# Optimization experiments

Hardware: AMD Instinct MI355X
Metric: run time of the kernel (lower is better)

The kernel has to match this reference:

```python
import jax, jax.numpy as jnp
import numpy as np


def setup_inputs() -> dict:
    key = jax.random.key(0)
    k1, k2, k3 = jax.random.split(key, 3)
    B, D = 16, 512
    lengths = np.array([1024 + 64 * i for i in range(B)], dtype=np.int64)  # ragged lens, max 1984
    N = int(lengths.sum())  # 24064 packed tokens
    h = jax.random.normal(k1, (N, D), dtype=jnp.float32)
    W = jax.random.normal(k2, (D, D), dtype=jnp.float32) / np.sqrt(D)
    b = jax.random.normal(k3, (D,), dtype=jnp.float32) * 0.01
    return {
        "h": h,
        "W": W,
        "b": b,
        "text_len_tensor": jnp.asarray(lengths),
        "max_len": int(lengths.max()),
    }


def reference(h, W, b, text_len_tensor, max_len):
    # h: [N, D] packed utterance features; text_len_tensor: [B] segment lengths.
    N, D = h.shape
    x = h @ W.T + b  # nn.Linear
    # Segment start offsets and padded gather indices [B, Lmax]
    offsets = jnp.concatenate(
        [jnp.zeros((1,), text_len_tensor.dtype), jnp.cumsum(text_len_tensor)[:-1]]
    )
    pos = jnp.arange(max_len)
    idx = offsets[:, None] + pos[None, :]
    mask = pos[None, :] < text_len_tensor[:, None]  # [B, Lmax] valid-token mask
    idx_c = jnp.clip(idx, 0, N - 1)
    z = h[idx_c] * mask[..., None]  # padded raw features  [B, Lmax, D]
    y = x[idx_c] * mask[..., None]  # padded projected     [B, Lmax, D]
    # Per-segment attention: scores[i, j] = z_i . y_j within each segment
    scores = jnp.einsum('bld,bmd->blm', z, y)
    scores = jnp.where(mask[:, None, :], scores, -1e9)  # mask invalid keys
    probs = jax.nn.softmax(scores, axis=-1)
    out = jnp.einsum('blm,bmd->bld', probs, z) * mask[..., None]
    # Scatter padded result back to packed layout (padding rows contribute zeros)
    ret = jnp.zeros_like(h).at[idx_c.reshape(-1)].add(out.reshape(-1, D))
    return ret
```

## Files before the change

kernel.cpp:

```cpp
#include <hip/hip_runtime.h>
#include <math.h>

#define D 512
#define AS1 __attribute__((address_space(1)))
#define AS3 __attribute__((address_space(3)))

typedef _Float16 f16x8 __attribute__((ext_vector_type(8)));
typedef float f32x4 __attribute__((ext_vector_type(4)));

__global__ __launch_bounds__(256) void transpose_kernel(
    const float* __restrict__ h, _Float16* __restrict__ zTb, int N)
{
    __shared__ float tile[64][65];
    const int t0 = blockIdx.x * 64;
    const int d0 = blockIdx.y * 64;
    const int tid = threadIdx.x;
    const int r0 = tid >> 4;
    const int c0 = (tid & 15) * 4;
    #pragma unroll
    for (int k = 0; k < 4; k++) {
        int r = r0 + k * 16;
        float4 v = *(const float4*)(h + (size_t)(t0 + r) * D + d0 + c0);
        tile[r][c0] = v.x; tile[r][c0+1] = v.y; tile[r][c0+2] = v.z; tile[r][c0+3] = v.w;
    }
    __syncthreads();
    const int g = (t0 >> 5) + (c0 >> 5);
    const int kk = c0 & 31;
    const int kg = kk >> 3;
    const int sub = kk & 7;
    #pragma unroll
    for (int k = 0; k < 4; k++) {
        int dd = d0 + r0 + k * 16;
        int kks = ((kg + (dd >> 1)) & 3) * 8 + sub;
        union { _Float16 hh[4]; uint2 u2; } pk;
        #pragma unroll
        for (int i = 0; i < 4; i++) pk.hh[i] = (_Float16)tile[c0 + i][r0 + k * 16];
        *(uint2*)(zTb + (size_t)g * 16384 + dd * 32 + kks) = pk.u2;
    }
}

__global__ __launch_bounds__(256) void linear_mfma(
    const float* __restrict__ h, const float* __restrict__ W,
    const float* __restrict__ bias, _Float16* __restrict__ x16, int N)
{
    __shared__ _Float16 sA[128 * 72];
    __shared__ _Float16 sB[128 * 72];
    const int tid  = threadIdx.x;
    const int m0 = blockIdx.x * 128;
    const int n0 = blockIdx.y * 128;
    const int wave = tid >> 6, lane = tid & 63;
    const int l15 = lane & 15, quad = lane >> 4;
    const int wm = (wave >> 1) * 64, wn = (wave & 1) * 64;

    f32x4 acc[4][4];
    #pragma unroll
    for (int mi = 0; mi < 4; mi++)
        #pragma unroll
        for (int ni = 0; ni < 4; ni++) acc[mi][ni] = (f32x4){0.f,0.f,0.f,0.f};

    for (int k0 = 0; k0 < D; k0 += 64) {
        __syncthreads();
        #pragma unroll
        for (int i = 0; i < 8; i++) {
            int idx = tid + 256 * i;
            int row = idx >> 4;
            int c4  = (idx & 15) * 4;
            float4 va = *(const float4*)(h + (size_t)(m0 + row) * D + k0 + c4);
            float4 vb = *(const float4*)(W + (size_t)(n0 + row) * D + k0 + c4);
            union { _Float16 hh[4]; uint2 u2; } pa, pb;
            pa.hh[0] = (_Float16)va.x; pa.hh[1] = (_Float16)va.y;
            pa.hh[2] = (_Float16)va.z; pa.hh[3] = (_Float16)va.w;
            pb.hh[0] = (_Float16)vb.x; pb.hh[1] = (_Float16)vb.y;
            pb.hh[2] = (_Float16)vb.z; pb.hh[3] = (_Float16)vb.w;
            *(uint2*)(sA + row * 72 + c4) = pa.u2;
            *(uint2*)(sB + row * 72 + c4) = pb.u2;
        }
        __syncthreads();
        #pragma unroll
        for (int kc = 0; kc < 2; kc++) {
            f16x8 a[4], b[4];
            #pragma unroll
            for (int mi = 0; mi < 4; mi++)
                a[mi] = *(const f16x8*)(sA + (wm + mi*16 + l15)*72 + kc*32 + quad*8);
            #pragma unroll
            for (int ni = 0; ni < 4; ni++)
                b[ni] = *(const f16x8*)(sB + (wn + ni*16 + l15)*72 + kc*32 + quad*8);
            #pragma unroll
            for (int mi = 0; mi < 4; mi++)
                #pragma unroll
                for (int ni = 0; ni < 4; ni++)
                    acc[mi][ni] = __builtin_amdgcn_mfma_f32_16x16x32_f16(a[mi], b[ni], acc[mi][ni], 0, 0, 0);
        }
    }
    float bv[4];
    #pragma unroll
    for (int ni = 0; ni < 4; ni++) bv[ni] = bias[n0 + wn + ni*16 + l15];
    #pragma unroll
    for (int mi = 0; mi < 4; mi++)
        #pragma unroll
        for (int ni = 0; ni < 4; ni++)
            #pragma unroll
            for (int r = 0; r < 4; r++) {
                int row = m0 + wm + mi*16 + quad*4 + r;
                x16[(size_t)row * D + n0 + wn + ni*16 + l15] = (_Float16)(acc[mi][ni][r] + bv[ni]);
            }
}

__global__ __launch_bounds__(256, 2) void attn9_kernel(
    const float* __restrict__ h, const _Float16* __restrict__ x16,
    const _Float16* __restrict__ zTb, const int* __restrict__ lens,
    float* __restrict__ out, int N, int B)
{
    __shared__ __align__(16) unsigned char smem[71168];
    _Float16* ybuf = (_Float16*)smem;
    _Float16* zbuf = (_Float16*)(smem + 33280);
    _Float16* pbuf = (_Float16*)(smem + 66048);

    const int is64 = (lens[1] == 0 && lens[3] == 0) ? 1 : 0;

    int seg = -1, tile = 0;
    if (B == 16) {
        const int xcd = blockIdx.x & 7;
        const int idx = blockIdx.x >> 3;
        const int sL = 15 - xcd, sS = xcd;
        const int LL = is64 ? lens[2 * sL] : lens[sL];
        const int LS = is64 ? lens[2 * sS] : lens[sS];
        const int ntL = (LL + 63) >> 6;
        const int ntS = (LS + 63) >> 6;
        if (idx < ntL)            { seg = sL; tile = idx; }
        else if (idx < ntL + ntS) { seg = sS; tile = idx - ntL; }
        else return;
    } else {
        int blk = blockIdx.x;
        int acc = 0;
        for (int t = 0; t < B; t++) {
            int s = B - 1 - t;
            int Ls = is64 ? lens[2 * s] : lens[s];
            int nt = (Ls + 63) >> 6;
            if (seg < 0 && blk < acc + nt) { seg = s; tile = blk - acc; }
            acc += nt;
        }
        if (seg < 0) return;
    }
    int off = 0;
    for (int t = 0; t < seg; t++) off += is64 ? lens[2 * t] : lens[t];
    const int len = is64 ? lens[2 * seg] : lens[seg];

    const int tid  = threadIdx.x;
    const int wv   = tid >> 6;
    const int lane = tid & 63;
    const int l15  = lane & 15;
    const int quad = lane >> 4;
    const int zcol = ((quad + (l15 >> 1)) & 3) * 8;

    f16x8 Qf[16];
    {
        int qr = off + tile * 64 + wv * 16 + l15;
        if (qr > N - 1) qr = N - 1;
        const float* hr = h + (size_t)qr * D;
        #pragma unroll
        for (int c = 0; c < 16; c++) {
            float4 u = *(const float4*)(hr + c * 32 + quad * 8);
            float4 v = *(const float4*)(hr + c * 32 + quad * 8 + 4);
            f16x8 q;
            q[0] = (_Float16)u.x; q[1] = (_Float16)u.y; q[2] = (_Float16)u.z; q[3] = (_Float16)u.w;
            q[4] = (_Float16)v.x; q[5] = (_Float16)v.y; q[6] = (_Float16)v.z; q[7] = (_Float16)v.w;
            Qf[c] = q;
        }
    }

    f32x4 O[32];
    #pragma unroll
    for (int f = 0; f < 32; f++) O[f] = (f32x4){0.f,0.f,0.f,0.f};
    float mR[4] = {-1e30f,-1e30f,-1e30f,-1e30f};
    float lR[4] = {0.f,0.f,0.f,0.f};

    _Float16* Pw = pbuf + wv * 640;
    const int nkb = (len + 31) >> 5;

    #pragma unroll
    for (int i = 0; i < 8; i++) {
        int r = wv * 8 + i;
        int gr = off + r; if (gr > N - 1) gr = N - 1;
        const _Float16* gsrc = x16 + (size_t)gr * D + lane * 8;
        __builtin_amdgcn_global_load_lds((const AS1 unsigned int*)gsrc,
                                         (AS3 unsigned int*)(ybuf + r * 520), 16, 0, 0);
    }
    __syncthreads();

    for (int kb = 0; kb < nkb; kb++) {
        const int j0 = kb * 32;

        {
            const _Float16* zsrc = zTb + (size_t)((off + j0) >> 5) * 16384;
            #pragma unroll
            for (int i = 0; i < 8; i++) {
                int half_off = (wv * 8 + i) * 512 + lane * 8;
                __builtin_amdgcn_global_load_lds((const AS1 unsigned int*)(zsrc + half_off),
                                                 (AS3 unsigned int*)(zbuf + half_off), 16, 0, 0);
            }
        }

        f32x4 s0 = (f32x4){0.f,0.f,0.f,0.f}, s1 = (f32x4){0.f,0.f,0.f,0.f};
        f32x4 s0b = (f32x4){0.f,0.f,0.f,0.f}, s1b = (f32x4){0.f,0.f,0.f,0.f};
        __builtin_amdgcn_s_setprio(1);
        #pragma unroll
        for (int c2 = 0; c2 < 8; c2++) {
            int ca = 2 * c2, cb = 2 * c2 + 1;
            f16x8 b0a = *(const f16x8*)(ybuf + l15 * 520 + ca * 32 + quad * 8);
            f16x8 b1a = *(const f16x8*)(ybuf + (16 + l15) * 520 + ca * 32 + quad * 8);
            f16x8 b0c = *(const f16x8*)(ybuf + l15 * 520 + cb * 32 + quad * 8);
            f16x8 b1c = *(const f16x8*)(ybuf + (16 + l15) * 520 + cb * 32 + quad * 8);
            s0  = __builtin_amdgcn_mfma_f32_16x16x32_f16(Qf[ca], b0a, s0,  0, 0, 0);
            s1  = __builtin_amdgcn_mfma_f32_16x16x32_f16(Qf[ca], b1a, s1,  0, 0, 0);
            s0b = __builtin_amdgcn_mfma_f32_16x16x32_f16(Qf[cb], b0c, s0b, 0, 0, 0);
            s1b = __builtin_amdgcn_mfma_f32_16x16x32_f16(Qf[cb], b1c, s1b, 0, 0, 0);
        }
        __builtin_amdgcn_s_setprio(0);
        s0 += s0b; s1 += s1b;
        const int kk0 = j0 + l15, kk1 = j0 + 16 + l15;
        #pragma unroll
        for (int r = 0; r < 4; r++) {
            if (kk0 >= len) s0[r] = -1e30f;
            if (kk1 >= len) s1[r] = -1e30f;
        }

        __syncthreads();

        if (kb + 1 < nkb) {
            const int jn = (kb + 1) * 32;
            #pragma unroll
            for (int i = 0; i < 8; i++) {
                int r = wv * 8 + i;
                int gr = off + jn + r; if (gr > N - 1) gr = N - 1;
                const _Float16* gsrc = x16 + (size_t)gr * D + lane * 8;
                __builtin_amdgcn_global_load_lds((const AS1 unsigned int*)gsrc,
                                                 (AS3 unsigned int*)(ybuf + r * 520), 16, 0, 0);
            }
        }

        float al[4];
        bool need = false;
        #pragma unroll
        for (int r = 0; r < 4; r++) {
            float t = fmaxf(s0[r], s1[r]);
            t = fmaxf(t, __shfl_xor(t, 1, 16));
            t = fmaxf(t, __shfl_xor(t, 2, 16));
            t = fmaxf(t, __shfl_xor(t, 4, 16));
            t = fmaxf(t, __shfl_xor(t, 8, 16));
            bool upd = (t > mR[r] + 8.0f);
            float mn = upd ? t : mR[r];
            al[r] = upd ? __expf(mR[r] - mn) : 1.0f;
            mR[r] = mn;
            float e0 = __expf(s0[r] - mn);
            float e1 = __expf(s1[r] - mn);
            float ps = e0 + e1;
            ps += __shfl_xor(ps, 1, 16);
            ps += __shfl_xor(ps, 2, 16);
            ps += __shfl_xor(ps, 4, 16);
            ps += __shfl_xor(ps, 8, 16);
            lR[r] = lR[r] * al[r] + ps;
            Pw[(quad * 4 + r) * 40 + l15]      = (_Float16)e0;
            Pw[(quad * 4 + r) * 40 + 16 + l15] = (_Float16)e1;
            need |= upd;
        }

        if (__ballot(need)) {
            f32x4 av; av[0] = al[0]; av[1] = al[1]; av[2] = al[2]; av[3] = al[3];
            #pragma unroll
            for (int f = 0; f < 32; f++) O[f] *= av;
        }
        f16x8 pf = *(const f16x8*)(Pw + l15 * 40 + quad * 8);

        __builtin_amdgcn_s_setprio(1);
        #pragma unroll
        for (int f = 0; f < 32; f++) {
            f16x8 zf = *(const f16x8*)(zbuf + (f * 16 + l15) * 32 + zcol);
            O[f] = __builtin_amdgcn_mfma_f32_16x16x32_f16(pf, zf, O[f], 0, 0, 0);
        }
        __builtin_amdgcn_s_setprio(0);

        __syncthreads();
    }

    float inv[4];
    #pragma unroll
    for (int r = 0; r < 4; r++) inv[r] = 1.0f / lR[r];
    #pragma unroll
    for (int r = 0; r < 4; r++) {
        int qloc = tile * 64 + wv * 16 + quad * 4 + r;
        if (qloc < len) {
            float* orow = out + (size_t)(off + qloc) * D + l15;
            #pragma unroll
            for (int f = 0; f < 32; f++) orow[f * 16] = O[f][r] * inv[r];
        }
    }
}

extern "C" void kernel_launch(void* const* d_in, const int* in_sizes, int n_in,
                              void* d_out, int out_size, void* d_ws, size_t ws_size,
                              hipStream_t stream) {
    const float* h    = (const float*)d_in[0];
    const float* W    = (const float*)d_in[1];
    const float* bias = (const float*)d_in[2];
    const int*   lens = (const int*)d_in[3];
    float* outp = (float*)d_out;

    const int N = in_sizes[0] / D;
    int B = in_sizes[3]; if (B > 16) B = 16;

    _Float16* x16 = (_Float16*)d_ws;
    _Float16* zTb = (_Float16*)((char*)d_ws + (size_t)N * D * 2);

    dim3 g2(N / 64, D / 64);
    transpose_kernel<<<g2, 256, 0, stream>>>(h, zTb, N);

    dim3 g1(N / 128, D / 128);
    linear_mfma<<<g1, 256, 0, stream>>>(h, W, bias, x16, N);

    const int nblk = N / 64 + B;
    attn9_kernel<<<nblk, 256, 0, stream>>>(h, x16, zTb, lens, outp, N, B);
}
```

Before: 338.6 us.

## Split attention waves into query-pair groups partitioned over feature halves

Restructures the attention kernel so each pair of waves shares 32 query rows, with each wave covering half of the 512-wide feature dimension. Every B-fragment loaded from LDS now feeds two MFMAs, which is meant to cut LDS read traffic for both the QK and PV products. Partial scores are exchanged through LDS and softmax state is shared through LDS buffers. This adds an extra barrier per key block and uses more shared memory, which could hurt occupancy or add sync stalls.

```diff
diff --git a/kernel.cpp b/kernel.cpp
--- a/kernel.cpp
+++ b/kernel.cpp
@@ -106,15 +106,16 @@
             }
 }
 
-__global__ __launch_bounds__(256, 2) void attn9_kernel(
+__global__ __launch_bounds__(256, 2) void attn12_kernel(
     const float* __restrict__ h, const _Float16* __restrict__ x16,
     const _Float16* __restrict__ zTb, const int* __restrict__ lens,
     float* __restrict__ out, int N, int B)
 {
-    __shared__ __align__(16) unsigned char smem[71168];
+    __shared__ __align__(16) unsigned char smem[76800];
     _Float16* ybuf = (_Float16*)smem;
-    _Float16* zbuf = (_Float16*)(smem + 33280);
-    _Float16* pbuf = (_Float16*)(smem + 66048);
+    _Float16* zbuf = (_Float16*)(smem + 34304);
+    float* albuf = (float*)(smem + 76288);
+    float* lbuf  = (float*)(smem + 76544);
 
     const int is64 = (lens[1] == 0 && lens[3] == 0) ? 1 : 0;
 
@@ -148,35 +149,38 @@
 
     const int tid  = threadIdx.x;
     const int wv   = tid >> 6;
+    const int g    = wv >> 1;
+    const int hh   = wv & 1;
     const int lane = tid & 63;
     const int l15  = lane & 15;
     const int quad = lane >> 4;
     const int zcol = ((quad + (l15 >> 1)) & 3) * 8;
-
-    f16x8 Qf[16];
-    {
-        int qr = off + tile * 64 + wv * 16 + l15;
+    const int nkb  = (len + 31) >> 5;
+
+    f16x8 Qf[2][8];
+    #pragma unroll
+    for (int ts = 0; ts < 2; ts++) {
+        int qr = off + tile * 64 + g * 32 + ts * 16 + l15;
         if (qr > N - 1) qr = N - 1;
-        const float* hr = h + (size_t)qr * D;
-        #pragma unroll
-        for (int c = 0; c < 16; c++) {
-            float4 u = *(const float4*)(hr + c * 32 + quad * 8);
-            float4 v = *(const float4*)(hr + c * 32 + quad * 8 + 4);
+        const float* hr = h + (size_t)qr * D + hh * 256;
+        #pragma unroll
+        for (int cc = 0; cc < 8; cc++) {
+            float4 u = *(const float4*)(hr + cc * 32 + quad * 8);
+            float4 v = *(const float4*)(hr + cc * 32 + quad * 8 + 4);
             f16x8 q;
             q[0] = (_Float16)u.x; q[1] = (_Float16)u.y; q[2] = (_Float16)u.z; q[3] = (_Float16)u.w;
             q[4] = (_Float16)v.x; q[5] = (_Float16)v.y; q[6] = (_Float16)v.z; q[7] = (_Float16)v.w;
-            Qf[c] = q;
-        }
-    }
-
-    f32x4 O[32];
-    #pragma unroll
-    for (int f = 0; f < 32; f++) O[f] = (f32x4){0.f,0.f,0.f,0.f};
+            Qf[ts][cc] = q;
+        }
+    }
+
+    f32x4 O[2][16];
+    #pragma unroll
+    for (int ts = 0; ts < 2; ts++)
+        #pragma unroll
+        for (int f = 0; f < 16; f++) O[ts][f] = (f32x4){0.f,0.f,0.f,0.f};
     float mR[4] = {-1e30f,-1e30f,-1e30f,-1e30f};
     float lR[4] = {0.f,0.f,0.f,0.f};
-
-    _Float16* Pw = pbuf + wv * 640;
-    const int nkb = (len + 31) >> 5;
 
     #pragma unroll
     for (int i = 0; i < 8; i++) {
@@ -184,47 +188,45 @@
         int gr = off + r; if (gr > N - 1) gr = N - 1;
         const _Float16* gsrc = x16 + (size_t)gr * D + lane * 8;
         __builtin_amdgcn_global_load_lds((const AS1 unsigned int*)gsrc,
-                                         (AS3 unsigned int*)(ybuf + r * 520), 16, 0, 0);
+                                         (AS3 unsigned int*)(ybuf + r * 536), 16, 0, 0);
     }
     __syncthreads();
 
     for (int kb = 0; kb < nkb; kb++) {
-        const int j0 = kb * 32;
-
         {
-            const _Float16* zsrc = zTb + (size_t)((off + j0) >> 5) * 16384;
+            const _Float16* zsrc = zTb + (size_t)((off + kb * 32) >> 5) * 16384;
             #pragma unroll
             for (int i = 0; i < 8; i++) {
-                int half_off = (wv * 8 + i) * 512 + lane * 8;
-                __builtin_amdgcn_global_load_lds((const AS1 unsigned int*)(zsrc + half_off),
-                                                 (AS3 unsigned int*)(zbuf + half_off), 16, 0, 0);
-            }
-        }
-
-        f32x4 s0 = (f32x4){0.f,0.f,0.f,0.f}, s1 = (f32x4){0.f,0.f,0.f,0.f};
-        f32x4 s0b = (f32x4){0.f,0.f,0.f,0.f}, s1b = (f32x4){0.f,0.f,0.f,0.f};
+                int co = (wv * 8 + i) * 512 + lane * 8;
+                __builtin_amdgcn_global_load_lds((const AS1 unsigned int*)(zsrc + co),
+                                                 (AS3 unsigned int*)(zbuf + co), 16, 0, 0);
+            }
+        }
+        f32x4 s[2][2];
+        #pragma unroll
+        for (int ts = 0; ts < 2; ts++)
+            #pragma unroll
+            for (int kt = 0; kt < 2; kt++) s[ts][kt] = (f32x4){0.f,0.f,0.f,0.f};
         __builtin_amdgcn_s_setprio(1);
         #pragma unroll
-        for (int c2 = 0; c2 < 8; c2++) {
-            int ca = 2 * c2, cb = 2 * c2 + 1;
-            f16x8 b0a = *(const f16x8*)(ybuf + l15 * 520 + ca * 32 + quad * 8);
-            f16x8 b1a = *(const f16x8*)(ybuf + (16 + l15) * 520 + ca * 32 + quad * 8);
-            f16x8 b0c = *(const f16x8*)(ybuf + l15 * 520 + cb * 32 + quad * 8);
-            f16x8 b1c = *(const f16x8*)(ybuf + (16 + l15) * 520 + cb * 32 + quad * 8);
-            s0  = __builtin_amdgcn_mfma_f32_16x16x32_f16(Qf[ca], b0a, s0,  0, 0, 0);
-            s1  = __builtin_amdgcn_mfma_f32_16x16x32_f16(Qf[ca], b1a, s1,  0, 0, 0);
-            s0b = __builtin_amdgcn_mfma_f32_16x16x32_f16(Qf[cb], b0c, s0b, 0, 0, 0);
-            s1b = __builtin_amdgcn_mfma_f32_16x16x32_f16(Qf[cb], b1c, s1b, 0, 0, 0);
+        for (int cc = 0; cc < 8; cc++) {
+            const _Float16* yb = ybuf + hh * 256 + cc * 32 + quad * 8;
+            f16x8 b0 = *(const f16x8*)(yb + l15 * 536);
+            f16x8 b1 = *(const f16x8*)(yb + (16 + l15) * 536);
+            s[0][0] = __builtin_amdgcn_mfma_f32_16x16x32_f16(Qf[0][cc], b0, s[0][0], 0, 0, 0);
+            s[1][0] = __builtin_amdgcn_mfma_f32_16x16x32_f16(Qf[1][cc], b0, s[1][0], 0, 0, 0);
+            s[0][1] = __builtin_amdgcn_mfma_f32_16x16x32_f16(Qf[0][cc], b1, s[0][1], 0, 0, 0);
+            s[1][1] = __builtin_amdgcn_mfma_f32_16x16x32_f16(Qf[1][cc], b1, s[1][1], 0, 0, 0);
         }
         __builtin_amdgcn_s_setprio(0);
-        s0 += s0b; s1 += s1b;
-        const int kk0 = j0 + l15, kk1 = j0 + 16 + l15;
-        #pragma unroll
-        for (int r = 0; r < 4; r++) {
-            if (kk0 >= len) s0[r] = -1e30f;
-            if (kk1 >= len) s1[r] = -1e30f;
-        }
-
+        {
+            float* sxw = (float*)(smem + 67072 + (size_t)(g * 2 + (1 - hh)) * 2304);
+            #pragma unroll
+            for (int kt = 0; kt < 2; kt++)
+                #pragma unroll
+                for (int r = 0; r < 4; r++)
+                    sxw[(quad * 4 + r) * 36 + kt * 16 + l15] = s[1 - hh][kt][r];
+        }
         __syncthreads();
 
         if (kb + 1 < nkb) {
@@ -235,64 +237,91 @@
                 int gr = off + jn + r; if (gr > N - 1) gr = N - 1;
                 const _Float16* gsrc = x16 + (size_t)gr * D + lane * 8;
                 __builtin_amdgcn_global_load_lds((const AS1 unsigned int*)gsrc,
-                                                 (AS3 unsigned int*)(ybuf + r * 520), 16, 0, 0);
-            }
-        }
-
-        float al[4];
-        bool need = false;
+                                                 (AS3 unsigned int*)(ybuf + r * 536), 16, 0, 0);
+            }
+        }
+        {
+            const float* sxr = (const float*)(smem + 67072 + (size_t)(g * 2 + hh) * 2304);
+            f32x4 sm[2];
+            #pragma unroll
+            for (int kt = 0; kt < 2; kt++)
+                #pragma unroll
+                for (int r = 0; r < 4; r++)
+                    sm[kt][r] = s[hh][kt][r] + sxr[(quad * 4 + r) * 36 + kt * 16 + l15];
+            const int kk0 = kb * 32 + l15, kk1 = kb * 32 + 16 + l15;
+            #pragma unroll
+            for (int r = 0; r < 4; r++) {
+                if (kk0 >= len) sm[0][r] = -1e30f;
+                if (kk1 >= len) sm[1][r] = -1e30f;
+            }
+            _Float16* pw = (_Float16*)(smem + 67072 + (size_t)(g * 2 + hh) * 2304);
+            #pragma unroll
+            for (int r = 0; r < 4; r++) {
+                float t = fmaxf(sm[0][r], sm[1][r]);
+                t = fmaxf(t, __shfl_xor(t, 1, 16));
+                t = fmaxf(t, __shfl_xor(t, 2, 16));
+                t = fmaxf(t, __shfl_xor(t, 4, 16));
+                t = fmaxf(t, __shfl_xor(t, 8, 16));
+                bool upd = (t > mR[r] + 8.0f);
+                float mn = upd ? t : mR[r];
+                float al = upd ? __expf(mR[r] - mn) : 1.0f;
+                mR[r] = mn;
+                float e0 = __expf(sm[0][r] - mn);
+                float e1 = __expf(sm[1][r] - mn);
+                float ps = e0 + e1;
+                ps += __shfl_xor(ps, 1, 16);
+                ps += __shfl_xor(ps, 2, 16);
+                ps += __shfl_xor(ps, 4, 16);
+                ps += __shfl_xor(ps, 8, 16);
+                lR[r] = lR[r] * al + ps;
+                pw[(quad * 4 + r) * 40 + l15]      = (_Float16)e0;
+                pw[(quad * 4 + r) * 40 + 16 + l15] = (_Float16)e1;
+                if (l15 == 0) {
+                    albuf[(g * 2 + hh) * 16 + quad * 4 + r] = al;
+                    if (kb == nkb - 1) lbuf[(g * 2 + hh) * 16 + quad * 4 + r] = 1.0f / lR[r];
+                }
+            }
+        }
+        __syncthreads();
+
+        {
+            const _Float16* p0 = (const _Float16*)(smem + 67072 + (size_t)(g * 2 + 0) * 2304);
+            const _Float16* p1 = (const _Float16*)(smem + 67072 + (size_t)(g * 2 + 1) * 2304);
+            f16x8 pa0 = *(const f16x8*)(p0 + l15 * 40 + quad * 8);
+            f16x8 pa1 = *(const f16x8*)(p1 + l15 * 40 + quad * 8);
+            f32x4 av0 = *(const f32x4*)(albuf + (g * 2 + 0) * 16 + quad * 4);
+            f32x4 av1 = *(const f32x4*)(albuf + (g * 2 + 1) * 16 + quad * 4);
+            bool upd = false;
+            #pragma unroll
+            for (int r = 0; r < 4; r++) upd |= (av0[r] != 1.0f) | (av1[r] != 1.0f);
+            if (__ballot(upd)) {
+                #pragma unroll
+                for (int f = 0; f < 16; f++) { O[0][f] *= av0; O[1][f] *= av1; }
+            }
+            const _Float16* zb = zbuf + (size_t)hh * 256 * 32 + zcol;
+            __builtin_amdgcn_s_setprio(1);
+            #pragma unroll
+            for (int f = 0; f < 16; f++) {
+                f16x8 zf = *(const f16x8*)(zb + (f * 16 + l15) * 32);
+                O[0][f] = __builtin_amdgcn_mfma_f32_16x16x32_f16(pa0, zf, O[0][f], 0, 0, 0);
+                O[1][f] = __builtin_amdgcn_mfma_f32_16x16x32_f16(pa1, zf, O[1][f], 0, 0, 0);
+            }
+            __builtin_amdgcn_s_setprio(0);
+        }
+        __syncthreads();
+    }
+
+    #pragma unroll
+    for (int ts = 0; ts < 2; ts++) {
+        f32x4 inv = *(const f32x4*)(lbuf + (g * 2 + ts) * 16 + quad * 4);
         #pragma unroll
         for (int r = 0; r < 4; r++) {
-            float t = fmaxf(s0[r], s1[r]);
-            t = fmaxf(t, __shfl_xor(t, 1, 16));
-            t = fmaxf(t, __shfl_xor(t, 2, 16));
-            t = fmaxf(t, __shfl_xor(t, 4, 16));
-            t = fmaxf(t, __shfl_xor(t, 8, 16));
-            bool upd = (t > mR[r] + 8.0f);
-            float mn = upd ? t : mR[r];
-            al[r] = upd ? __expf(mR[r] - mn) : 1.0f;
-            mR[r] = mn;
-            float e0 = __expf(s0[r] - mn);
-            float e1 = __expf(s1[r] - mn);
-            float ps = e0 + e1;
-            ps += __shfl_xor(ps, 1, 16);
-            ps += __shfl_xor(ps, 2, 16);
-            ps += __shfl_xor(ps, 4, 16);
-            ps += __shfl_xor(ps, 8, 16);
-            lR[r] = lR[r] * al[r] + ps;
-            Pw[(quad * 4 + r) * 40 + l15]      = (_Float16)e0;
-            Pw[(quad * 4 + r) * 40 + 16 + l15] = (_Float16)e1;
-            need |= upd;
-        }
-
-        if (__ballot(need)) {
-            f32x4 av; av[0] = al[0]; av[1] = al[1]; av[2] = al[2]; av[3] = al[3];
-            #pragma unroll
-            for (int f = 0; f < 32; f++) O[f] *= av;
-        }
-        f16x8 pf = *(const f16x8*)(Pw + l15 * 40 + quad * 8);
-
-        __builtin_amdgcn_s_setprio(1);
-        #pragma unroll
-        for (int f = 0; f < 32; f++) {
-            f16x8 zf = *(const f16x8*)(zbuf + (f * 16 + l15) * 32 + zcol);
-            O[f] = __builtin_amdgcn_mfma_f32_16x16x32_f16(pf, zf, O[f], 0, 0, 0);
-        }
-        __builtin_amdgcn_s_setprio(0);
-
-        __syncthreads();
-    }
-
-    float inv[4];
-    #pragma unroll
-    for (int r = 0; r < 4; r++) inv[r] = 1.0f / lR[r];
-    #pragma unroll
-    for (int r = 0; r < 4; r++) {
-        int qloc = tile * 64 + wv * 16 + quad * 4 + r;
-        if (qloc < len) {
-            float* orow = out + (size_t)(off + qloc) * D + l15;
-            #pragma unroll
-            for (int f = 0; f < 32; f++) orow[f * 16] = O[f][r] * inv[r];
+            int qloc = tile * 64 + g * 32 + ts * 16 + quad * 4 + r;
+            if (qloc < len) {
+                float* orow = out + (size_t)(off + qloc) * D + hh * 256 + l15;
+                #pragma unroll
+                for (int f = 0; f < 16; f++) orow[f * 16] = O[ts][f][r] * inv[r];
+            }
         }
     }
 }
@@ -319,5 +348,5 @@
     linear_mfma<<<g1, 256, 0, stream>>>(h, W, bias, x16, N);
 
     const int nblk = N / 64 + B;
-    attn9_kernel<<<nblk, 256, 0, stream>>>(h, x16, zTb, lens, outp, N, B);
+    attn12_kernel<<<nblk, 256, 0, stream>>>(h, x16, zTb, lens, outp, N, B);
 }
```

After: 562.0 us. +66.0%, slower.

## Double-buffer Y and Z tiles in LDS for attention kernel

Applied to the files above, without the earlier changes.

The attention kernel now keeps two LDS buffers each for the projected key tile and the transposed value tile. The next block's loads are issued before the current block's score MFMAs, so global-to-LDS transfers overlap compute and the mid-loop barrier is removed. LDS use roughly doubles to about 134 KB and launch bounds fall from two blocks per CU to one, which cuts occupancy and latency hiding across blocks. The score accumulation also drops its split dual-accumulator chain for a single chain per output tile.

```diff
diff --git a/kernel.cpp b/kernel.cpp
--- a/kernel.cpp
+++ b/kernel.cpp
@@ -106,15 +106,12 @@
             }
 }
 
-__global__ __launch_bounds__(256, 2) void attn9_kernel(
+__global__ __launch_bounds__(256, 1) void attn13_kernel(
     const float* __restrict__ h, const _Float16* __restrict__ x16,
     const _Float16* __restrict__ zTb, const int* __restrict__ lens,
     float* __restrict__ out, int N, int B)
 {
-    __shared__ __align__(16) unsigned char smem[71168];
-    _Float16* ybuf = (_Float16*)smem;
-    _Float16* zbuf = (_Float16*)(smem + 33280);
-    _Float16* pbuf = (_Float16*)(smem + 66048);
+    __shared__ __align__(16) unsigned char smem[137216];
 
     const int is64 = (lens[1] == 0 && lens[3] == 0) ? 1 : 0;
 
@@ -152,6 +149,7 @@
     const int l15  = lane & 15;
     const int quad = lane >> 4;
     const int zcol = ((quad + (l15 >> 1)) & 3) * 8;
+    const int nkb  = (len + 31) >> 5;
 
     f16x8 Qf[16];
     {
@@ -175,68 +173,70 @@
     float mR[4] = {-1e30f,-1e30f,-1e30f,-1e30f};
     float lR[4] = {0.f,0.f,0.f,0.f};
 
-    _Float16* Pw = pbuf + wv * 640;
-    const int nkb = (len + 31) >> 5;
-
-    #pragma unroll
-    for (int i = 0; i < 8; i++) {
-        int r = wv * 8 + i;
-        int gr = off + r; if (gr > N - 1) gr = N - 1;
-        const _Float16* gsrc = x16 + (size_t)gr * D + lane * 8;
-        __builtin_amdgcn_global_load_lds((const AS1 unsigned int*)gsrc,
-                                         (AS3 unsigned int*)(ybuf + r * 520), 16, 0, 0);
+    _Float16* Pw = (_Float16*)(smem + 132096) + wv * 640;
+
+    {
+        #pragma unroll
+        for (int i = 0; i < 8; i++) {
+            int r = wv * 8 + i;
+            int gr = off + r; if (gr > N - 1) gr = N - 1;
+            const _Float16* gsrc = x16 + (size_t)gr * D + lane * 8;
+            __builtin_amdgcn_global_load_lds((const AS1 unsigned int*)gsrc,
+                                             (AS3 unsigned int*)((_Float16*)smem + r * 520), 16, 0, 0);
+        }
+        const _Float16* zsrc = zTb + (size_t)(off >> 5) * 16384;
+        _Float16* zdst = (_Float16*)(smem + 66560);
+        #pragma unroll
+        for (int i = 0; i < 8; i++) {
+            int co = (wv * 8 + i) * 512 + lane * 8;
+            __builtin_amdgcn_global_load_lds((const AS1 unsigned int*)(zsrc + co),
+                                             (AS3 unsigned int*)(zdst + co), 16, 0, 0);
+        }
     }
     __syncthreads();
 
     for (int kb = 0; kb < nkb; kb++) {
-        const int j0 = kb * 32;
-
-        {
-            const _Float16* zsrc = zTb + (size_t)((off + j0) >> 5) * 16384;
-            #pragma unroll
-            for (int i = 0; i < 8; i++) {
-                int half_off = (wv * 8 + i) * 512 + lane * 8;
-                __builtin_amdgcn_global_load_lds((const AS1 unsigned int*)(zsrc + half_off),
-                                                 (AS3 unsigned int*)(zbuf + half_off), 16, 0, 0);
-            }
-        }
-
-        f32x4 s0 = (f32x4){0.f,0.f,0.f,0.f}, s1 = (f32x4){0.f,0.f,0.f,0.f};
-        f32x4 s0b = (f32x4){0.f,0.f,0.f,0.f}, s1b = (f32x4){0.f,0.f,0.f,0.f};
-        __builtin_amdgcn_s_setprio(1);
-        #pragma unroll
-        for (int c2 = 0; c2 < 8; c2++) {
-            int ca = 2 * c2, cb = 2 * c2 + 1;
-            f16x8 b0a = *(const f16x8*)(ybuf + l15 * 520 + ca * 32 + quad * 8);
-            f16x8 b1a = *(const f16x8*)(ybuf + (16 + l15) * 520 + ca * 32 + quad * 8);
-            f16x8 b0c = *(const f16x8*)(ybuf + l15 * 520 + cb * 32 + quad * 8);
-            f16x8 b1c = *(const f16x8*)(ybuf + (16 + l15) * 520 + cb * 32 + quad * 8);
-            s0  = __builtin_amdgcn_mfma_f32_16x16x32_f16(Qf[ca], b0a, s0,  0, 0, 0);
-            s1  = __builtin_amdgcn_mfma_f32_16x16x32_f16(Qf[ca], b1a, s1,  0, 0, 0);
-            s0b = __builtin_amdgcn_mfma_f32_16x16x32_f16(Qf[cb], b0c, s0b, 0, 0, 0);
-            s1b = __builtin_amdgcn_mfma_f32_16x16x32_f16(Qf[cb], b1c, s1b, 0, 0, 0);
-        }
-        __builtin_amdgcn_s_setprio(0);
-        s0 += s0b; s1 += s1b;
-        const int kk0 = j0 + l15, kk1 = j0 + 16 + l15;
-        #pragma unroll
-        for (int r = 0; r < 4; r++) {
-            if (kk0 >= len) s0[r] = -1e30f;
-            if (kk1 >= len) s1[r] = -1e30f;
-        }
-
-        __syncthreads();
+        const int cur = kb & 1;
+        const int nxt = cur ^ 1;
+        _Float16* ybuf = (_Float16*)(smem + (size_t)cur * 33280);
+        _Float16* zbuf = (_Float16*)(smem + 66560 + (size_t)cur * 32768);
 
         if (kb + 1 < nkb) {
             const int jn = (kb + 1) * 32;
+            _Float16* ydst = (_Float16*)(smem + (size_t)nxt * 33280);
             #pragma unroll
             for (int i = 0; i < 8; i++) {
                 int r = wv * 8 + i;
                 int gr = off + jn + r; if (gr > N - 1) gr = N - 1;
                 const _Float16* gsrc = x16 + (size_t)gr * D + lane * 8;
                 __builtin_amdgcn_global_load_lds((const AS1 unsigned int*)gsrc,
-                                                 (AS3 unsigned int*)(ybuf + r * 520), 16, 0, 0);
+                                                 (AS3 unsigned int*)(ydst + r * 520), 16, 0, 0);
             }
+            const _Float16* zsrc = zTb + (size_t)((off + jn) >> 5) * 16384;
+            _Float16* zdst = (_Float16*)(smem + 66560 + (size_t)nxt * 32768);
+            #pragma unroll
+            for (int i = 0; i < 8; i++) {
+                int co = (wv * 8 + i) * 512 + lane * 8;
+                __builtin_amdgcn_global_load_lds((const AS1 unsigned int*)(zsrc + co),
+                                                 (AS3 unsigned int*)(zdst + co), 16, 0, 0);
+            }
+        }
+
+        f32x4 s0 = (f32x4){0.f,0.f,0.f,0.f}, s1 = (f32x4){0.f,0.f,0.f,0.f};
+        __builtin_amdgcn_s_setprio(1);
+        #pragma unroll
+        for (int c = 0; c < 16; c++) {
+            f16x8 b0 = *(const f16x8*)(ybuf + l15 * 520 + c * 32 + quad * 8);
+            f16x8 b1 = *(const f16x8*)(ybuf + (16 + l15) * 520 + c * 32 + quad * 8);
+            s0 = __builtin_amdgcn_mfma_f32_16x16x32_f16(Qf[c], b0, s0, 0, 0, 0);
+            s1 = __builtin_amdgcn_mfma_f32_16x16x32_f16(Qf[c], b1, s1, 0, 0, 0);
+        }
+        __builtin_amdgcn_s_setprio(0);
+        const int kk0 = kb * 32 + l15, kk1 = kb * 32 + 16 + l15;
+        #pragma unroll
+        for (int r = 0; r < 4; r++) {
+            if (kk0 >= len) s0[r] = -1e30f;
+            if (kk1 >= len) s1[r] = -1e30f;
         }
 
         float al[4];
@@ -319,5 +319,5 @@
     linear_mfma<<<g1, 256, 0, stream>>>(h, W, bias, x16, N);
 
     const int nblk = N / 64 + B;
-    attn9_kernel<<<nblk, 256, 0, stream>>>(h, x16, zTb, lens, outp, N, B);
+    attn13_kernel<<<nblk, 256, 0, stream>>>(h, x16, zTb, lens, outp, N, B);
 }
```

After: 428.7 us. +26.6%, slower.
